# Optimization experiments

Hardware: AMD Instinct MI355X
Metric: run time of the kernel (lower is better)

## Reference

```python
import jax, jax.numpy as jnp
import numpy as np

N, E = 50000, 800000
IN, MAP, H, O = 256, 64, 4, 64
LEAKY_SLOPE = 0.2


def setup_inputs() -> dict:
    key = jax.random.key(0)
    ks = jax.random.split(key, 12)
    x = jax.random.normal(ks[0], (N, IN), dtype=jnp.float32)
    src = jax.random.randint(ks[1], (E,), 0, N, dtype=jnp.int32)
    dst = jax.random.randint(ks[2], (E,), 0, N, dtype=jnp.int32)
    s = 1.0 / np.sqrt(IN)
    W_gat = jax.random.normal(ks[3], (IN, H * O), dtype=jnp.float32) * s
    attn_l = jax.random.normal(ks[4], (H, O), dtype=jnp.float32) * 0.1
    attn_r = jax.random.normal(ks[5], (H, O), dtype=jnp.float32) * 0.1
    gate_m_W = jax.random.normal(ks[6], (IN, MAP), dtype=jnp.float32) * s
    gate_m_b = jnp.zeros((MAP,), dtype=jnp.float32)
    gate_fn_W = jax.random.normal(ks[7], (2 * IN + MAP, H), dtype=jnp.float32) * (1.0 / np.sqrt(2 * IN + MAP))
    gate_fn_b = jnp.zeros((H,), dtype=jnp.float32)
    merge_W = jax.random.normal(ks[8], (IN + O, O), dtype=jnp.float32) * (1.0 / np.sqrt(IN + O))
    merge_b = jnp.zeros((O,), dtype=jnp.float32)
    return {"x": x, "src": src, "dst": dst, "W_gat": W_gat, "attn_l": attn_l,
            "attn_r": attn_r, "gate_m_W": gate_m_W, "gate_m_b": gate_m_b,
            "gate_fn_W": gate_fn_W, "gate_fn_b": gate_fn_b,
            "merge_W": merge_W, "merge_b": merge_b}


def _forward(x, src, dst, W_gat, attn_l, attn_r, gate_m_W, gate_m_b,
             gate_fn_W, gate_fn_b, merge_W, merge_b):
    n = x.shape[0]
    # --- gate branch: gspmm mean of x, gspmm max of linear_z over in-neighbors ---
    deg = jax.ops.segment_sum(jnp.ones_like(dst, dtype=x.dtype), dst, num_segments=n)
    mean_z = jax.ops.segment_sum(x[src], dst, num_segments=n) / jnp.maximum(deg, 1.0)[:, None]
    z = x @ gate_m_W + gate_m_b  # [N, MAP]
    max_z = jax.ops.segment_max(z[src], dst, num_segments=n)
    max_z = jnp.where(deg[:, None] > 0, max_z, 0.0)  # empty neighborhoods -> 0
    nft = jnp.concatenate([x, max_z, mean_z], axis=1)  # [N, 2*IN+MAP]
    gate = jax.nn.sigmoid(nft @ gate_fn_W + gate_fn_b)  # [N, H]
    # --- GATConv ---
    feat = (x @ W_gat).reshape(n, H, O)  # [N, H, O]
    el = jnp.einsum('nho,ho->nh', feat, attn_l)
    er = jnp.einsum('nho,ho->nh', feat, attn_r)
    e = jax.nn.leaky_relu(el[src] + er[dst], negative_slope=LEAKY_SLOPE)  # [E, H]
    m = jax.ops.segment_max(e, dst, num_segments=n)  # [N, H]
    m = jnp.where(jnp.isfinite(m), m, 0.0)
    ex = jnp.exp(e - m[dst])  # [E, H]
    s = jax.ops.segment_sum(ex, dst, num_segments=n)  # [N, H]
    alpha = ex / jnp.maximum(s[dst], 1e-16)  # [E, H]
    attn_out = jax.ops.segment_sum(feat[src] * alpha[:, :, None], dst, num_segments=n)  # [N, H, O]
    # --- gated merge ---
    gated = (gate[:, :, None] * attn_out).mean(axis=1)  # [N, O]
    merge = jnp.concatenate([x, gated], axis=1) @ merge_W + merge_b  # [N, O]
    return merge


def reference(x, src, dst, W_gat, attn_l, attn_r, gate_m_W, gate_m_b,
              gate_fn_W, gate_fn_b, merge_W, merge_b):
    return _forward(x, src, dst, W_gat, attn_l, attn_r, gate_m_W, gate_m_b,
                    gate_fn_W, gate_fn_b, merge_W, merge_b)
```

## Files before the change

kernel.cpp:

```cpp
#include <hip/hip_runtime.h>
#include <math.h>

#define NN 50000
#define NE 800000
#define LEAKY 0.2f
#define NT 26
#define CAP 96
#define NBT (8 * NT * 64)
#define NRB 3125
#define PACK_BLKS 6250
#define BT_BLKS 54
#define INIT_BLKS 196

typedef short bf16x8 __attribute__((ext_vector_type(8)));
typedef float f32x4 __attribute__((ext_vector_type(4)));
typedef float f32x2 __attribute__((ext_vector_type(2)));

__device__ __forceinline__ unsigned short f2bf(float f) {
  unsigned u = __float_as_uint(f);
  u += 0x7fffu + ((u >> 16) & 1u);
  return (unsigned short)(u >> 16);
}
__device__ __forceinline__ float leaky(float v) { return v > 0.0f ? v : LEAKY * v; }
__device__ __forceinline__ float rlf(float v, int l) {
  return __uint_as_float(__builtin_amdgcn_readlane(__float_as_uint(v), l));
}
__device__ __forceinline__ int rli(int v, int l) {
  return __builtin_amdgcn_readlane(v, l);
}

#if defined(__has_builtin)
#if __has_builtin(__builtin_amdgcn_cvt_pk_f32_fp8) && \
    __has_builtin(__builtin_amdgcn_cvt_pk_fp8_f32) && \
    __has_builtin(__builtin_amdgcn_cvt_f32_fp8)
#define FP8_HW 1
#endif
#endif

#ifdef FP8_HW
__device__ __forceinline__ unsigned char f2fp8(float v) {
  return (unsigned char)(__builtin_amdgcn_cvt_pk_fp8_f32(v, v, 0u, false) & 0xFF);
}
__device__ __forceinline__ f32x2 fp8x2_lo(unsigned int v) {
  return __builtin_amdgcn_cvt_pk_f32_fp8(v, false);
}
__device__ __forceinline__ f32x2 fp8x2_hi(unsigned int v) {
  return __builtin_amdgcn_cvt_pk_f32_fp8(v, true);
}
__device__ __forceinline__ float fp8one(unsigned int v) {
  return __builtin_amdgcn_cvt_f32_fp8(v, 0);
}
#else
__device__ __forceinline__ unsigned char f2fp8(float f) {
  unsigned u = __float_as_uint(f);
  unsigned s = (u >> 31) << 7;
  unsigned a = u & 0x7FFFFFFFu;
  if (a >= 0x43E00000u) return (unsigned char)(s | 0x7E);
  if (a < 0x3C800000u) {
    float m = __uint_as_float(a) * 512.0f;
    int q = (int)(m + 0.5f); if (q > 7) q = 7;
    return (unsigned char)(s | q);
  }
  a += 0x7FFFFu + ((a >> 20) & 1);
  unsigned e = ((a >> 23) & 0xFF) - 120;
  if (e > 15) return (unsigned char)(s | 0x7E);
  return (unsigned char)(s | (e << 3) | ((a >> 20) & 7));
}
__device__ __forceinline__ float fp8dec1(unsigned b) {
  unsigned s = (b & 0x80u) << 24;
  unsigned em = b & 0x7Fu;
  unsigned e4 = em >> 3, m3 = em & 7;
  float v = e4 ? __uint_as_float(((e4 + 120) << 23) | (m3 << 20))
               : (float)m3 * 0.001953125f;
  return __uint_as_float(__float_as_uint(v) ^ s);
}
__device__ __forceinline__ f32x2 fp8x2_lo(unsigned int v) {
  f32x2 r; r[0] = fp8dec1(v & 0xFF); r[1] = fp8dec1((v >> 8) & 0xFF); return r;
}
__device__ __forceinline__ f32x2 fp8x2_hi(unsigned int v) {
  f32x2 r; r[0] = fp8dec1((v >> 16) & 0xFF); r[1] = fp8dec1((v >> 24) & 0xFF); return r;
}
__device__ __forceinline__ float fp8one(unsigned int v) { return fp8dec1(v & 0xFF); }
#endif

__device__ __forceinline__ float panel_w(int col, int k,
    const float* W_gat, const float* gate_m_W, const float* merge_W,
    const float* gate_fn_W) {
  if (col < 256)      return W_gat[k * 256 + (col & 3) * 64 + (col >> 2)];
  else if (col < 320) return gate_m_W[k * 64 + (col - 256)];
  else if (col < 384) return merge_W[k * 64 + (col - 320)];
  else if (col < 388) return gate_fn_W[k * 4 + (col - 384)];
  else if (col < 392) return gate_fn_W[(320 + k) * 4 + (col - 388)];
  return 0.0f;
}

__global__ __launch_bounds__(256) void k_prep(
    const float* __restrict__ x, const float* __restrict__ W_gat,
    const float* __restrict__ gate_m_W, const float* __restrict__ merge_W,
    const float* __restrict__ gate_fn_W,
    unsigned short* __restrict__ xf, unsigned short* __restrict__ Btf,
    unsigned short* __restrict__ mWf,
    int* __restrict__ cursor, unsigned char* __restrict__ zq,
    float* __restrict__ epay) {
  int b = blockIdx.x, tid = threadIdx.x;
  if (b < PACK_BLKS) {
    int gid = b * 256 + tid;
    int rowblk = gid >> 9;
    int rem = gid & 511;
    int kq = rem >> 6, lane = rem & 63;
    int m = lane & 15, kg = lane >> 4;
    const float* p = x + (size_t)(rowblk * 16 + m) * 256 + kq * 32 + kg * 8;
    float4 fa = *(const float4*)p;
    float4 fb = *(const float4*)(p + 4);
    ushort4 o0, o1;
    o0.x = f2bf(fa.x); o0.y = f2bf(fa.y); o0.z = f2bf(fa.z); o0.w = f2bf(fa.w);
    o1.x = f2bf(fb.x); o1.y = f2bf(fb.y); o1.z = f2bf(fb.z); o1.w = f2bf(fb.w);
    ushort4* dst = (ushort4*)(xf + (size_t)gid * 8);
    dst[0] = o0; dst[1] = o1;
  } else if (b < PACK_BLKS + BT_BLKS) {
    int idx = (b - PACK_BLKS) * 256 + tid;
    if (idx < NBT) {
      int kq = idx / (NT * 64);
      int rem = idx - kq * (NT * 64);
      int t = rem >> 6, lane = rem & 63;
      int col = t * 16 + (lane & 15);
      int k = kq * 32 + (lane >> 4) * 8;
      unsigned short* o = Btf + (size_t)idx * 8;
#pragma unroll
      for (int i = 0; i < 8; ++i)
        o[i] = f2bf(panel_w(col, k + i, W_gat, gate_m_W, merge_W, gate_fn_W));
    } else if (idx < NBT + 512) {
      int idx2 = idx - NBT;
      int kq = idx2 >> 8;
      int rem = idx2 & 255;
      int t = rem >> 6, lane = rem & 63;
      int col = t * 16 + (lane & 15);
      int k = kq * 32 + ((lane >> 4) & 3) * 8;
      unsigned short* o = mWf + (size_t)idx2 * 8;
#pragma unroll
      for (int i = 0; i < 8; ++i)
        o[i] = f2bf(merge_W[(size_t)(256 + k + i) * 64 + col]);
    }
  } else {
    int i = (b - PACK_BLKS - BT_BLKS) * 256 + tid;
    if (i < NN) cursor[i] = 0;
    if (b == PACK_BLKS + BT_BLKS) {
      if (tid < 64) zq[(size_t)NN * 64 + tid] = 0xFE;
      if (tid < 8) epay[(size_t)NN * 8 + tid] = 0.0f;
    }
  }
}

__global__ void k_scatter(const int* __restrict__ src, const int* __restrict__ dst,
                          int* __restrict__ cursor, unsigned short* __restrict__ csr_src) {
  int e = blockIdx.x * 256 + threadIdx.x;
  if (e < NE) {
    int n = dst[e];
    int pos = atomicAdd(&cursor[n], 1);
    if (pos < CAP) csr_src[n * CAP + pos] = (unsigned short)src[e];
  }
}

__global__ __launch_bounds__(256, 2) void k_gemm_mfma(
    const unsigned short* __restrict__ xf, const unsigned short* __restrict__ Btf,
    const float* __restrict__ gate_m_b,
    const float* __restrict__ attn_l, const float* __restrict__ attn_r,
    unsigned char* __restrict__ featq, unsigned char* __restrict__ zq,
    float* __restrict__ xm, float* __restrict__ gx, float* __restrict__ epay,
    float* __restrict__ erv) {
  __shared__ float els[64][4][2];
  __shared__ float ers[64][4][2];
  int lane = threadIdx.x & 63;
  int wave = threadIdx.x >> 6;
  int rowHalf = wave >> 1, colHalf = wave & 1;
  int rowB = blockIdx.x * 64;
  int row0 = rowB + rowHalf * 32;
  int t0 = colHalf * 13;
  int m = lane & 15, kg = lane >> 4;
  f32x4 zero = {0.f, 0.f, 0.f, 0.f};
  f32x4 acc[2][13];
#pragma unroll
  for (int g = 0; g < 2; ++g)
#pragma unroll
    for (int t = 0; t < 13; ++t) acc[g][t] = zero;

  const unsigned short* aB0 = xf + ((size_t)((blockIdx.x * 4 + rowHalf * 2) * 8) * 64 + lane) * 8;
  const unsigned short* aB1 = aB0 + (size_t)8 * 64 * 8;
  const unsigned short* bB = Btf + (size_t)(t0 * 64 + lane) * 8;

  bf16x8 aC0, aC1, aN0, aN1, bC[13], bN[13];
  aC0 = *(const bf16x8*)(aB0);
  aC1 = *(const bf16x8*)(aB1);
#pragma unroll
  for (int t = 0; t < 13; ++t)
    bC[t] = *(const bf16x8*)(bB + (size_t)t * 512);
#pragma unroll 1
  for (int kq = 0; kq < 8; kq += 2) {
    aN0 = *(const bf16x8*)(aB0 + (size_t)(kq + 1) * 512);
    aN1 = *(const bf16x8*)(aB1 + (size_t)(kq + 1) * 512);
#pragma unroll
    for (int t = 0; t < 13; ++t)
      bN[t] = *(const bf16x8*)(bB + ((size_t)(kq + 1) * NT + t) * 512);
#pragma unroll
    for (int t = 0; t < 13; ++t)
      acc[0][t] = __builtin_amdgcn_mfma_f32_16x16x32_bf16(aC0, bC[t], acc[0][t], 0, 0, 0);
#pragma unroll
    for (int t = 0; t < 13; ++t)
      acc[1][t] = __builtin_amdgcn_mfma_f32_16x16x32_bf16(aC1, bC[t], acc[1][t], 0, 0, 0);
    int kq2 = kq + 2 < 8 ? kq + 2 : 7;
    aC0 = *(const bf16x8*)(aB0 + (size_t)kq2 * 512);
    aC1 = *(const bf16x8*)(aB1 + (size_t)kq2 * 512);
#pragma unroll
    for (int t = 0; t < 13; ++t)
      bC[t] = *(const bf16x8*)(bB + ((size_t)kq2 * NT + t) * 512);
#pragma unroll
    for (int t = 0; t < 13; ++t)
      acc[0][t] = __builtin_amdgcn_mfma_f32_16x16x32_bf16(aN0, bN[t], acc[0][t], 0, 0, 0);
#pragma unroll
    for (int t = 0; t < 13; ++t)
      acc[1][t] = __builtin_amdgcn_mfma_f32_16x16x32_bf16(aN1, bN[t], acc[1][t], 0, 0, 0);
  }

  int h = m & 3, od = m >> 2;
  float elp[2][4] = {{0,0,0,0},{0,0,0,0}}, erp[2][4] = {{0,0,0,0},{0,0,0,0}};
#pragma unroll
  for (int t = 0; t < 13; ++t) {
    if ((t0 + t) * 16 < 256) {
      int o = (t0 + t) * 4 + od;
      float al = attn_l[h * 64 + o];
      float ar = attn_r[h * 64 + o];
#pragma unroll
      for (int g = 0; g < 2; ++g)
#pragma unroll
        for (int r = 0; r < 4; ++r) {
          elp[g][r] += acc[g][t][r] * al;
          erp[g][r] += acc[g][t][r] * ar;
        }
    }
  }
#pragma unroll
  for (int g = 0; g < 2; ++g)
#pragma unroll
    for (int r = 0; r < 4; ++r) {
      elp[g][r] += __shfl_xor(elp[g][r], 4, 64); elp[g][r] += __shfl_xor(elp[g][r], 8, 64);
      erp[g][r] += __shfl_xor(erp[g][r], 4, 64); erp[g][r] += __shfl_xor(erp[g][r], 8, 64);
    }
  if (m < 4) {
#pragma unroll
    for (int g = 0; g < 2; ++g)
#pragma unroll
      for (int r = 0; r < 4; ++r) {
        els[rowHalf * 32 + g * 16 + kg * 4 + r][m][colHalf] = elp[g][r];
        ers[rowHalf * 32 + g * 16 + kg * 4 + r][m][colHalf] = erp[g][r];
      }
  }

#pragma unroll
  for (int g = 0; g < 2; ++g) {
    if (colHalf == 0) {
#pragma unroll
      for (int r = 0; r < 4; ++r) {
        int row = row0 + g * 16 + kg * 4 + r;
        if (row >= NN) continue;
#pragma unroll
        for (int t = 0; t < 13; ++t)
          featq[(size_t)row * 256 + t * 16 + m] = f2fp8(acc[g][t][r]);
      }
    } else {
#pragma unroll
      for (int r = 0; r < 4; ++r) {
        int row = row0 + g * 16 + kg * 4 + r;
        if (row >= NN) continue;
#pragma unroll
        for (int t = 0; t < 3; ++t)
          featq[(size_t)row * 256 + 208 + t * 16 + m] = f2fp8(acc[g][t][r]);
#pragma unroll
        for (int t = 3; t < 7; ++t) {
          int cc = (t - 3) * 16 + m;
          zq[(size_t)row * 64 + cc] = f2fp8(acc[g][t][r] + gate_m_b[cc]);
        }
#pragma unroll
        for (int t = 7; t < 11; ++t)
          xm[(size_t)row * 64 + (t - 7) * 16 + m] = acc[g][t][r];
        if (m < 4) gx[(size_t)row * 4 + m] = acc[g][11][r];
        else if (m < 8) epay[(size_t)row * 8 + (m - 4) * 2 + 1] = acc[g][11][r];
      }
    }
  }
  __syncthreads();
  int tid = threadIdx.x;
  {
    int rr = tid >> 2, h2 = tid & 3;
    int row = rowB + rr;
    if (row < NN) {
      epay[(size_t)row * 8 + h2 * 2] = els[rr][h2][0] + els[rr][h2][1];
      erv[(size_t)row * 4 + h2] = ers[rr][h2][0] + ers[rr][h2][1];
    }
  }
}

__global__ __launch_bounds__(256) void k_node(
    const unsigned char* __restrict__ zq, const unsigned char* __restrict__ featq,
    const float* __restrict__ epay, const float* __restrict__ er,
    const float* __restrict__ gx,
    const int* __restrict__ cursor, const unsigned short* __restrict__ csr_src,
    const float* __restrict__ gate_fn_W, const float* __restrict__ gate_fn_b,
    const unsigned short* __restrict__ mWf, const float* __restrict__ xm,
    const float* __restrict__ merge_b, float* __restrict__ out) {
  __shared__ float WzT[4][64];
  __shared__ float pbuf[4][16][4];
  __shared__ unsigned short gLDS[16][72];
  int tid = threadIdx.x;
  {
    int c = tid >> 2, h = tid & 3;
    WzT[h][c] = gate_fn_W[(256 + c) * 4 + h];
  }
  __syncthreads();

  int lane = tid & 63, wave = tid >> 6;
  int hh = lane >> 4, le = lane & 15;
  int nodeBase = blockIdx.x * 16 + wave * 4;
#pragma unroll 1
  for (int i = 0; i < 4; ++i) {
    int node = nodeBase + i;
    int deg = cursor[node]; if (deg > CAP) deg = CAP;
    float gated = 0.0f;
    if (deg > 0) {
      int rs = node * CAP, re = rs + deg;
      float er_h = er[(size_t)node * 4 + hh];
      float a0 = 0, a1 = 0, a2 = 0, a3 = 0;
      float psum = 0, usum = 0;
      float mz = -INFINITY;
      for (int j0 = rs; j0 < re; j0 += 16) {
        int jj = j0 + le;
        bool valid = jj < re;
        int s_l = valid ? (int)csr_src[jj] : NN;
        float2 eu = *(const float2*)(epay + ((size_t)(unsigned)s_l << 3) + hh * 2);
        float p = valid ? __expf(leaky(eu.x + er_h)) : 0.0f;
        psum += p;
        usum += valid ? eu.y : 0.0f;
        pbuf[wave][le][hh] = p;
#pragma unroll
        for (int e2 = 0; e2 < 16; ++e2) {
          int s = rli(s_l, e2);
          float4 pv = *(const float4*)pbuf[wave][e2];
          unsigned int fv = *(const unsigned int*)(featq + ((size_t)(unsigned)s << 8) + lane * 4);
          unsigned int zv = zq[((size_t)(unsigned)s << 6) + lane];
          f32x2 lo = fp8x2_lo(fv);
          f32x2 hi = fp8x2_hi(fv);
          a0 += pv.x * lo[0];
          a1 += pv.y * lo[1];
          a2 += pv.z * hi[0];
          a3 += pv.w * hi[1];
          mz = fmaxf(mz, fp8one(zv));
        }
      }
#pragma unroll
      for (int off = 1; off < 16; off <<= 1) {
        psum += __shfl_xor(psum, off, 64);
        usum += __shfl_xor(usum, off, 64);
      }
      float s0 = rlf(psum, 0),  s1 = rlf(psum, 16);
      float s2 = rlf(psum, 32), s3 = rlf(psum, 48);
      float su0 = rlf(usum, 0),  su1 = rlf(usum, 16);
      float su2 = rlf(usum, 32), su3 = rlf(usum, 48);

      float g[4];
#pragma unroll
      for (int h = 0; h < 4; ++h) {
        float t = mz * WzT[h][lane];
#pragma unroll
        for (int off = 32; off; off >>= 1) t += __shfl_xor(t, off, 64);
        g[h] = t;
      }
      float inv_deg = 1.0f / (float)deg;
      float4 gx4 = *(const float4*)(gx + (size_t)node * 4);
      float g0 = 1.0f / (1.0f + __expf(-(g[0] + gx4.x + su0 * inv_deg + gate_fn_b[0])));
      float g1 = 1.0f / (1.0f + __expf(-(g[1] + gx4.y + su1 * inv_deg + gate_fn_b[1])));
      float g2 = 1.0f / (1.0f + __expf(-(g[2] + gx4.z + su2 * inv_deg + gate_fn_b[2])));
      float g3 = 1.0f / (1.0f + __expf(-(g[3] + gx4.w + su3 * inv_deg + gate_fn_b[3])));
      gated = 0.25f * (g0 * a0 / s0 + g1 * a1 / s1 + g2 * a2 / s2 + g3 * a3 / s3);
    }
    gLDS[wave * 4 + i][lane] = f2bf(gated);
  }
  __syncthreads();

  int m = lane & 15, kg = lane >> 4;
  f32x4 acc = {0.f, 0.f, 0.f, 0.f};
#pragma unroll
  for (int kq = 0; kq < 2; ++kq) {
    bf16x8 a = *(const bf16x8*)(&gLDS[m][kq * 32 + kg * 8]);
    bf16x8 b = *(const bf16x8*)(mWf + (((size_t)kq * 4 + wave) * 64 + lane) * 8);
    acc = __builtin_amdgcn_mfma_f32_16x16x32_bf16(a, b, acc, 0, 0, 0);
  }
  int c = wave * 16 + m;
  float mb = merge_b[c];
#pragma unroll
  for (int r = 0; r < 4; ++r) {
    int row = blockIdx.x * 16 + kg * 4 + r;
    out[(size_t)row * 64 + c] = acc[r] + xm[(size_t)row * 64 + c] + mb;
  }
}

extern "C" void kernel_launch(void* const* d_in, const int* in_sizes, int n_in,
                              void* d_out, int out_size, void* d_ws, size_t ws_size,
                              hipStream_t stream) {
  const float* x         = (const float*)d_in[0];
  const int*   src       = (const int*)d_in[1];
  const int*   dst       = (const int*)d_in[2];
  const float* W_gat     = (const float*)d_in[3];
  const float* attn_l    = (const float*)d_in[4];
  const float* attn_r    = (const float*)d_in[5];
  const float* gate_m_W  = (const float*)d_in[6];
  const float* gate_m_b  = (const float*)d_in[7];
  const float* gate_fn_W = (const float*)d_in[8];
  const float* gate_fn_b = (const float*)d_in[9];
  const float* merge_W   = (const float*)d_in[10];
  const float* merge_b   = (const float*)d_in[11];
  float* out = (float*)d_out;

  char* ws = (char*)d_ws;
  size_t off = 0;
  auto alloc = [&](size_t bytes) -> void* {
    off = (off + 255) & ~(size_t)255;
    void* p = ws + off;
    off += bytes;
    return p;
  };
  int* cursor    = (int*)alloc((size_t)NN * 4);
  unsigned short* csr_src = (unsigned short*)alloc((size_t)NN * CAP * 2);
  float* epay = (float*)alloc((size_t)(NN + 1) * 8 * 4);
  float* er   = (float*)alloc((size_t)NN * 4 * 4);
  float* gx   = (float*)alloc((size_t)NN * 4 * 4);
  float* xm   = (float*)alloc((size_t)NN * 64 * 4);
  unsigned char* zq    = (unsigned char*)alloc((size_t)(NN + 1) * 64);
  unsigned char* featq = (unsigned char*)alloc((size_t)(NN + 1) * 256);
  unsigned short* xf     = (unsigned short*)alloc((size_t)(NRB + 4) * 512 * 8 * 2);
  unsigned short* Btf    = (unsigned short*)alloc((size_t)NBT * 8 * 2);
  unsigned short* mWf    = (unsigned short*)alloc((size_t)512 * 8 * 2);

  k_prep<<<PACK_BLKS + BT_BLKS + INIT_BLKS, 256, 0, stream>>>(
      x, W_gat, gate_m_W, merge_W, gate_fn_W, xf, Btf, mWf, cursor, zq, epay);
  k_scatter<<<(NE + 255) / 256, 256, 0, stream>>>(src, dst, cursor, csr_src);
  k_gemm_mfma<<<(NN + 63) / 64, 256, 0, stream>>>(xf, Btf, gate_m_b, attn_l, attn_r,
                                                  featq, zq, xm, gx, epay, er);
  k_node<<<NN / 16, 256, 0, stream>>>(zq, featq, epay, er, gx, cursor, csr_src,
                                      gate_fn_W, gate_fn_b, mWf, xm, merge_b, out);
}
```

Baseline: 247.5 us.

## Split wave into four edge groups with wide feature loads in node aggregation

```diff
diff --git a/kernel.cpp b/kernel.cpp
--- a/kernel.cpp
+++ b/kernel.cpp
@@ -101,7 +101,7 @@
     unsigned short* __restrict__ xf, unsigned short* __restrict__ Btf,
     unsigned short* __restrict__ mWf,
     int* __restrict__ cursor, unsigned char* __restrict__ zq,
-    float* __restrict__ epay) {
+    float* __restrict__ epay, unsigned char* __restrict__ featq) {
   int b = blockIdx.x, tid = threadIdx.x;
   if (b < PACK_BLKS) {
     int gid = b * 256 + tid;
@@ -147,6 +147,7 @@
     if (b == PACK_BLKS + BT_BLKS) {
       if (tid < 64) zq[(size_t)NN * 64 + tid] = 0xFE;
       if (tid < 8) epay[(size_t)NN * 8 + tid] = 0.0f;
+      featq[(size_t)NN * 256 + tid] = 0;
     }
   }
 }
@@ -318,41 +319,52 @@
   __syncthreads();
 
   int lane = tid & 63, wave = tid >> 6;
-  int hh = lane >> 4, le = lane & 15;
+  int hh = lane >> 4;
+  int lq = lane & 15;
   int nodeBase = blockIdx.x * 16 + wave * 4;
 #pragma unroll 1
   for (int i = 0; i < 4; ++i) {
     int node = nodeBase + i;
     int deg = cursor[node]; if (deg > CAP) deg = CAP;
-    float gated = 0.0f;
+    float go0 = 0.f, go1 = 0.f, go2 = 0.f, go3 = 0.f;
     if (deg > 0) {
       int rs = node * CAP, re = rs + deg;
       float er_h = er[(size_t)node * 4 + hh];
-      float a0 = 0, a1 = 0, a2 = 0, a3 = 0;
-      float psum = 0, usum = 0;
-      float mz = -INFINITY;
+      f32x2 A[8];
+#pragma unroll
+      for (int j = 0; j < 8; ++j) A[j] = (f32x2){0.f, 0.f};
+      f32x2 M0 = {-INFINITY, -INFINITY};
+      f32x2 M1 = {-INFINITY, -INFINITY};
+      float psum = 0.f, usum = 0.f;
       for (int j0 = rs; j0 < re; j0 += 16) {
-        int jj = j0 + le;
+        int jj = j0 + lq;
         bool valid = jj < re;
         int s_l = valid ? (int)csr_src[jj] : NN;
         float2 eu = *(const float2*)(epay + ((size_t)(unsigned)s_l << 3) + hh * 2);
         float p = valid ? __expf(leaky(eu.x + er_h)) : 0.0f;
         psum += p;
-        usum += valid ? eu.y : 0.0f;
-        pbuf[wave][le][hh] = p;
-#pragma unroll
-        for (int e2 = 0; e2 < 16; ++e2) {
-          int s = rli(s_l, e2);
-          float4 pv = *(const float4*)pbuf[wave][e2];
-          unsigned int fv = *(const unsigned int*)(featq + ((size_t)(unsigned)s << 8) + lane * 4);
-          unsigned int zv = zq[((size_t)(unsigned)s << 6) + lane];
-          f32x2 lo = fp8x2_lo(fv);
-          f32x2 hi = fp8x2_hi(fv);
-          a0 += pv.x * lo[0];
-          a1 += pv.y * lo[1];
-          a2 += pv.z * hi[0];
-          a3 += pv.w * hi[1];
-          mz = fmaxf(mz, fp8one(zv));
+        usum += eu.y;
+        pbuf[wave][lq][hh] = p;
+#pragma unroll
+        for (int it = 0; it < 4; ++it) {
+          int es = it * 4 + hh;
+          int s = __shfl(s_l, es, 64);
+          float4 pv = *(const float4*)pbuf[wave][es];
+          uint4 fv = *(const uint4*)(featq + ((size_t)(unsigned)s << 8) + lq * 16);
+          unsigned int zv = *(const unsigned int*)(zq + ((size_t)(unsigned)s << 6) + lq * 4);
+          f32x2 p01 = {pv.x, pv.y};
+          f32x2 p23 = {pv.z, pv.w};
+          A[0] += p01 * fp8x2_lo(fv.x);
+          A[1] += p23 * fp8x2_hi(fv.x);
+          A[2] += p01 * fp8x2_lo(fv.y);
+          A[3] += p23 * fp8x2_hi(fv.y);
+          A[4] += p01 * fp8x2_lo(fv.z);
+          A[5] += p23 * fp8x2_hi(fv.z);
+          A[6] += p01 * fp8x2_lo(fv.w);
+          A[7] += p23 * fp8x2_hi(fv.w);
+          f32x2 zlo = fp8x2_lo(zv), zhi = fp8x2_hi(zv);
+          M0[0] = fmaxf(M0[0], zlo[0]); M0[1] = fmaxf(M0[1], zlo[1]);
+          M1[0] = fmaxf(M1[0], zhi[0]); M1[1] = fmaxf(M1[1], zhi[1]);
         }
       }
 #pragma unroll
@@ -364,24 +376,46 @@
       float s2 = rlf(psum, 32), s3 = rlf(psum, 48);
       float su0 = rlf(usum, 0),  su1 = rlf(usum, 16);
       float su2 = rlf(usum, 32), su3 = rlf(usum, 48);
-
-      float g[4];
+#pragma unroll
+      for (int j = 0; j < 8; ++j) {
+        A[j][0] += __shfl_xor(A[j][0], 16, 64); A[j][1] += __shfl_xor(A[j][1], 16, 64);
+        A[j][0] += __shfl_xor(A[j][0], 32, 64); A[j][1] += __shfl_xor(A[j][1], 32, 64);
+      }
+      M0[0] = fmaxf(M0[0], __shfl_xor(M0[0], 16, 64));
+      M0[1] = fmaxf(M0[1], __shfl_xor(M0[1], 16, 64));
+      M1[0] = fmaxf(M1[0], __shfl_xor(M1[0], 16, 64));
+      M1[1] = fmaxf(M1[1], __shfl_xor(M1[1], 16, 64));
+      M0[0] = fmaxf(M0[0], __shfl_xor(M0[0], 32, 64));
+      M0[1] = fmaxf(M0[1], __shfl_xor(M0[1], 32, 64));
+      M1[0] = fmaxf(M1[0], __shfl_xor(M1[0], 32, 64));
+      M1[1] = fmaxf(M1[1], __shfl_xor(M1[1], 32, 64));
+      float gq[4];
 #pragma unroll
       for (int h = 0; h < 4; ++h) {
-        float t = mz * WzT[h][lane];
-#pragma unroll
-        for (int off = 32; off; off >>= 1) t += __shfl_xor(t, off, 64);
-        g[h] = t;
+        float4 wz = *(const float4*)&WzT[h][lq * 4];
+        float t = M0[0] * wz.x + M0[1] * wz.y + M1[0] * wz.z + M1[1] * wz.w;
+#pragma unroll
+        for (int off = 1; off < 16; off <<= 1) t += __shfl_xor(t, off, 64);
+        gq[h] = t;
       }
       float inv_deg = 1.0f / (float)deg;
       float4 gx4 = *(const float4*)(gx + (size_t)node * 4);
-      float g0 = 1.0f / (1.0f + __expf(-(g[0] + gx4.x + su0 * inv_deg + gate_fn_b[0])));
-      float g1 = 1.0f / (1.0f + __expf(-(g[1] + gx4.y + su1 * inv_deg + gate_fn_b[1])));
-      float g2 = 1.0f / (1.0f + __expf(-(g[2] + gx4.z + su2 * inv_deg + gate_fn_b[2])));
-      float g3 = 1.0f / (1.0f + __expf(-(g[3] + gx4.w + su3 * inv_deg + gate_fn_b[3])));
-      gated = 0.25f * (g0 * a0 / s0 + g1 * a1 / s1 + g2 * a2 / s2 + g3 * a3 / s3);
-    }
-    gLDS[wave * 4 + i][lane] = f2bf(gated);
+      float g0 = 1.0f / (1.0f + __expf(-(gq[0] + gx4.x + su0 * inv_deg + gate_fn_b[0])));
+      float g1 = 1.0f / (1.0f + __expf(-(gq[1] + gx4.y + su1 * inv_deg + gate_fn_b[1])));
+      float g2 = 1.0f / (1.0f + __expf(-(gq[2] + gx4.z + su2 * inv_deg + gate_fn_b[2])));
+      float g3 = 1.0f / (1.0f + __expf(-(gq[3] + gx4.w + su3 * inv_deg + gate_fn_b[3])));
+      float r0 = 0.25f * g0 / s0, r1 = 0.25f * g1 / s1;
+      float r2 = 0.25f * g2 / s2, r3 = 0.25f * g3 / s3;
+      go0 = r0 * A[0][0] + r1 * A[0][1] + r2 * A[1][0] + r3 * A[1][1];
+      go1 = r0 * A[2][0] + r1 * A[2][1] + r2 * A[3][0] + r3 * A[3][1];
+      go2 = r0 * A[4][0] + r1 * A[4][1] + r2 * A[5][0] + r3 * A[5][1];
+      go3 = r0 * A[6][0] + r1 * A[6][1] + r2 * A[7][0] + r3 * A[7][1];
+    }
+    if (hh == 0) {
+      ushort4 gw;
+      gw.x = f2bf(go0); gw.y = f2bf(go1); gw.z = f2bf(go2); gw.w = f2bf(go3);
+      *(ushort4*)&gLDS[wave * 4 + i][lq * 4] = gw;
+    }
   }
   __syncthreads();
 
@@ -440,7 +474,7 @@
   unsigned short* mWf    = (unsigned short*)alloc((size_t)512 * 8 * 2);
 
   k_prep<<<PACK_BLKS + BT_BLKS + INIT_BLKS, 256, 0, stream>>>(
-      x, W_gat, gate_m_W, merge_W, gate_fn_W, xf, Btf, mWf, cursor, zq, epay);
+      x, W_gat, gate_m_W, merge_W, gate_fn_W, xf, Btf, mWf, cursor, zq, epay, featq);
   k_scatter<<<(NE + 255) / 256, 256, 0, stream>>>(src, dst, cursor, csr_src);
   k_gemm_mfma<<<(NN + 63) / 64, 256, 0, stream>>>(xf, Btf, gate_m_b, attn_l, attn_r,
                                                   featq, zq, xm, gx, epay, er);
```

After: 258.3 us. 1.04x slower.
